# Kernel tuning notes

Measured on AMD Instinct MI355X. Metric: run time of the kernel, lower is better.

## Reference

```python
import jax, jax.numpy as jnp
import numpy as np

IN_FEATURE = 256
OUT_FEATURE = 128
ALPHA = 0.5  # LeakyReLU negative slope
NEG_BIG = -9e15


def setup_inputs() -> dict:
    key = jax.random.key(0)
    k1, k2, k3, k4 = jax.random.split(key, 4)
    N = 8192
    x = jax.random.normal(k1, (N, IN_FEATURE), dtype=jnp.float32)
    adj = jax.random.randint(k2, (N, N), 0, 2, dtype=jnp.int32)
    stdv = 1.0 / np.sqrt(OUT_FEATURE)
    W = jax.random.uniform(k3, (IN_FEATURE, OUT_FEATURE), dtype=jnp.float32,
                           minval=-stdv, maxval=stdv)
    a = jax.random.uniform(k4, (2 * OUT_FEATURE, 1), dtype=jnp.float32,
                           minval=-stdv, maxval=stdv)
    return {"input": x, "adj": adj, "W": W, "a": a}


def reference(input, adj, W, a):
    # h: [N, F_out]
    h = input @ W
    # Additive attention: cat([h_i, h_j]) @ a == h_i @ a1 + h_j @ a2
    a1 = a[:OUT_FEATURE, 0]   # [F_out]
    a2 = a[OUT_FEATURE:, 0]   # [F_out]
    f1 = h @ a1               # [N]  (row / source contribution)
    f2 = h @ a2               # [N]  (col / target contribution)
    e = jax.nn.leaky_relu(f1[:, None] + f2[None, :], negative_slope=ALPHA)  # [N, N]
    scores = jnp.where(adj > 0, e, NEG_BIG)
    attention = jax.nn.softmax(scores, axis=1)  # [N, N]
    h_prime = attention @ h                     # [N, F_out]
    return jax.nn.elu(h_prime)
```

## Files before the change

### kernel.cpp

```cpp
#include <hip/hip_runtime.h>

#define N_NODES 8192
#define IN_F 256
#define OUT_F 128
#define ALPHA 0.5f
#define JC 8
#define KCHUNK 1024
#define RK 32
#define ROUNDS 32

using short8 = __attribute__((ext_vector_type(8))) short;
using f32x4  = __attribute__((ext_vector_type(4))) float;

__device__ __forceinline__ unsigned int f2bf(float f){
  unsigned int u = __float_as_uint(f);
  u += 0x7fffu + ((u >> 16) & 1u);
  return u >> 16;
}

__device__ __forceinline__ void gld16(const void* g, void* l){
  __builtin_amdgcn_global_load_lds(
      (const __attribute__((address_space(1))) unsigned int*)g,
      (__attribute__((address_space(3))) unsigned int*)l, 16, 0, 0);
}

__global__ __launch_bounds__(256) void k_h(const float* __restrict__ x,
                                           const float* __restrict__ W,
                                           float* __restrict__ h){
  __shared__ float xs[16*IN_F];
  const int tid = threadIdx.x;
  const int r0 = blockIdx.x * 16;
  const float4* xg = (const float4*)(x + (size_t)r0*IN_F);
  float4* xl = (float4*)xs;
  #pragma unroll
  for(int i=0;i<4;i++) xl[tid + i*256] = xg[tid + i*256];
  __syncthreads();
  const int wave = tid >> 6, lane = tid & 63;
  float2 acc[4];
  #pragma unroll
  for(int j=0;j<4;j++){ acc[j].x = 0.f; acc[j].y = 0.f; }
  const float2* Wp = (const float2*)W;
  for(int k4=0;k4<IN_F;k4+=4){
    float4 xq[4];
    #pragma unroll
    for(int j=0;j<4;j++) xq[j] = *(const float4*)&xs[(wave*4+j)*IN_F + k4];
    #pragma unroll
    for(int kk=0;kk<4;kk++){
      float2 wv = Wp[(size_t)(k4+kk)*64 + lane];
      #pragma unroll
      for(int j=0;j<4;j++){
        float xv = kk==0?xq[j].x : kk==1?xq[j].y : kk==2?xq[j].z : xq[j].w;
        acc[j].x += xv*wv.x; acc[j].y += xv*wv.y;
      }
    }
  }
  #pragma unroll
  for(int j=0;j<4;j++)
    *(float2*)(h + (size_t)(r0 + wave*4 + j)*OUT_F + lane*2) = acc[j];
}

__global__ __launch_bounds__(256) void k_f(const float* __restrict__ h,
                                           const float* __restrict__ a,
                                           float* __restrict__ f1,
                                           float* __restrict__ f2){
  const int wave = threadIdx.x >> 6, lane = threadIdx.x & 63;
  const int row = blockIdx.x*4 + wave;
  float2 hv = ((const float2*)(h + (size_t)row*OUT_F))[lane];
  float2 a1 = ((const float2*)a)[lane];
  float2 a2 = ((const float2*)(a + OUT_F))[lane];
  float s1 = hv.x*a1.x + hv.y*a1.y;
  float s2 = hv.x*a2.x + hv.y*a2.y;
  #pragma unroll
  for(int off=32; off; off>>=1){
    s1 += __shfl_down(s1, off);
    s2 += __shfl_down(s2, off);
  }
  if(lane == 0){ f1[row] = s1; f2[row] = s2; }
}

#define LDW 132
__global__ __launch_bounds__(256) void k_pack(const float* __restrict__ h,
                                              unsigned short* __restrict__ P){
  __shared__ float ld[32*LDW];
  const int tid = threadIdx.x;
  const int kb = blockIdx.x, j0 = kb*32;
  #pragma unroll
  for(int i=0;i<4;i++){
    int idx = tid + i*256;
    int row = idx >> 5, c4 = (idx & 31)*4;
    *(float4*)&ld[row*LDW + c4] = *(const float4*)(h + (size_t)(j0+row)*OUT_F + c4);
  }
  __syncthreads();
  #pragma unroll
  for(int i=0;i<2;i++){
    int o = tid*2 + i;
    int c = o >> 6, lane = o & 63;
    int q = lane >> 4, n = lane & 15;
    short8 v;
    #pragma unroll
    for(int t=0;t<8;t++) v[t] = (short)f2bf(ld[(q*8+t)*LDW + c*16 + n]);
    *(short8*)(P + ((size_t)(kb*8 + c)*64 + lane)*8) = v;
  }
}

__global__ __launch_bounds__(256, 2) void k_attn(const int* __restrict__ adj,
    const unsigned short* __restrict__ P,
    const float* __restrict__ f1, const float* __restrict__ f2,
    float* __restrict__ part, float* __restrict__ denp){
  __shared__ __align__(16) char Alds[2][16384];
  __shared__ __align__(16) char Blds[2][8192];
  __shared__ float f2s[KCHUNK];
  __shared__ float f1s[128];
  const int tid = threadIdx.x;
  const int wave = tid >> 6, lane = tid & 63;
  const int m = lane & 15, q = lane >> 4;
  const int jc = blockIdx.x;
  const int r0b = blockIdx.y * 128;
  const int jb = jc * KCHUNK;

  ((float4*)f2s)[tid] = ((const float4*)(f2 + jb))[tid];
  if(tid < 128) f1s[tid] = f1[r0b + tid];

  const int g = (lane & 7) ^ (lane >> 3);
  const char* asrc[4];
  #pragma unroll
  for(int i=0;i<4;i++){
    int rowid = (wave*4 + i)*8 + (lane >> 3);
    asrc[i] = (const char*)(adj + (size_t)(r0b + rowid)*N_NODES + jb) + g*16;
  }
  const char* bsrc[2];
  #pragma unroll
  for(int i=0;i<2;i++)
    bsrc[i] = (const char*)P + (size_t)jc*ROUNDS*8192 + ((size_t)(wave*2+i)*64 + lane)*16;

  auto issue_dma = [&](int rd, int buf){
    #pragma unroll
    for(int i=0;i<4;i++)
      gld16(asrc[i] + (size_t)rd*128, Alds[buf] + (wave*4+i)*1024 + lane*16);
    #pragma unroll
    for(int i=0;i<2;i++)
      gld16(bsrc[i] + (size_t)rd*8192, Blds[buf] + (wave*2+i)*1024 + lane*16);
  };

  issue_dma(0, 0);

  f32x4 acc0[8], acc1[8];
  #pragma unroll
  for(int c=0;c<8;c++){ acc0[c] = (f32x4){0,0,0,0}; acc1[c] = (f32x4){0,0,0,0}; }
  float den0 = 0.f, den1 = 0.f;

  const int rg0 = wave*32 + m;
  const int xr = m & 7;
  const int s0 = (q*2) ^ xr, s1 = s0 ^ 1;

  __syncthreads();
  const float rf1a = f1s[rg0];
  const float rf1b = f1s[rg0 + 16];

  auto wcalc = [&](int4 alo, int4 ahi, float4 fva, float4 fvb,
                   float rf1, float& den) -> short8 {
    short8 af; float t, w;
    #define WE(slot, av, fv)                              \
      t = rf1 + (fv); t = fmaxf(t, ALPHA*t);              \
      w = ((av) > 0) ? __expf(t) : 0.f;                   \
      den += w; af[slot] = (short)f2bf(w);
    WE(0,alo.x,fva.x) WE(1,alo.y,fva.y) WE(2,alo.z,fva.z) WE(3,alo.w,fva.w)
    WE(4,ahi.x,fvb.x) WE(5,ahi.y,fvb.y) WE(6,ahi.z,fvb.z) WE(7,ahi.w,fvb.w)
    #undef WE
    return af;
  };

  for(int rd=0; rd<ROUNDS; rd++){
    const int buf = rd & 1;
    if(rd+1 < ROUNDS) issue_dma(rd+1, buf ^ 1);
    const int4* Arow0 = (const int4*)(Alds[buf] + rg0*128);
    const int4* Arow1 = (const int4*)(Alds[buf] + (rg0+16)*128);
    int4 alo0 = Arow0[s0], ahi0 = Arow0[s1];
    int4 alo1 = Arow1[s0], ahi1 = Arow1[s1];
    float4 fva = *(const float4*)(f2s + rd*RK + q*8);
    float4 fvb = *(const float4*)(f2s + rd*RK + q*8 + 4);
    short8 af0 = wcalc(alo0, ahi0, fva, fvb, rf1a, den0);
    short8 af1 = wcalc(alo1, ahi1, fva, fvb, rf1b, den1);
    const short8* Bl = (const short8*)(Blds[buf]) + lane;
    #pragma unroll
    for(int c=0;c<8;c++){
      short8 Bf = Bl[c*64];
      acc0[c] = __builtin_amdgcn_mfma_f32_16x16x32_bf16(af0, Bf, acc0[c], 0,0,0);
      acc1[c] = __builtin_amdgcn_mfma_f32_16x16x32_bf16(af1, Bf, acc1[c], 0,0,0);
    }
    __syncthreads();
  }

  den0 += __shfl_down(den0, 32); den0 += __shfl_down(den0, 16);
  den1 += __shfl_down(den1, 32); den1 += __shfl_down(den1, 16);
  const int r0w = r0b + wave*32;
  if(lane < 16){
    denp[(size_t)jc*N_NODES + r0w + lane]      = den0;
    denp[(size_t)jc*N_NODES + r0w + 16 + lane] = den1;
  }
  float* pp = part + (size_t)jc*N_NODES*OUT_F;
  #pragma unroll
  for(int c=0;c<8;c++){
    #pragma unroll
    for(int reg=0;reg<4;reg++){
      pp[(size_t)(r0w + q*4 + reg)*OUT_F      + c*16 + m] = acc0[c][reg];
      pp[(size_t)(r0w + 16 + q*4 + reg)*OUT_F + c*16 + m] = acc1[c][reg];
    }
  }
}

__global__ __launch_bounds__(256) void k_out(const float* __restrict__ part,
    const float* __restrict__ denp, float* __restrict__ out){
  const int idx = blockIdx.x*256 + threadIdx.x;
  const int r = idx >> 7;
  float v = 0.f, d = 0.f;
  #pragma unroll
  for(int p=0;p<JC;p++){
    v += part[(size_t)p*N_NODES*OUT_F + idx];
    d += denp[(size_t)p*N_NODES + r];
  }
  v /= d;
  out[idx] = v > 0.f ? v : (__expf(v) - 1.f);
}

extern "C" void kernel_launch(void* const* d_in, const int* in_sizes, int n_in,
                              void* d_out, int out_size, void* d_ws, size_t ws_size,
                              hipStream_t stream){
  const float* x   = (const float*)d_in[0];
  const int*   adj = (const int*)d_in[1];
  const float* W   = (const float*)d_in[2];
  const float* a   = (const float*)d_in[3];
  char* ws = (char*)d_ws;
  float* h            = (float*)ws;
  unsigned short* P   = (unsigned short*)(ws + (4u<<20));
  float* f1           = (float*)(ws + (6u<<20));
  float* f2           = (float*)(ws + (6u<<20) + (32u<<10));
  float* part         = (float*)(ws + (8u<<20));
  float* denp         = (float*)(ws + (40u<<20));
  float* out          = (float*)d_out;

  k_h<<<512, 256, 0, stream>>>(x, W, h);
  k_f<<<2048, 256, 0, stream>>>(h, a, f1, f2);
  k_pack<<<256, 256, 0, stream>>>(h, P);
  k_attn<<<dim3(JC,64), 256, 0, stream>>>(adj, P, f1, f2, part, denp);
  k_out<<<(N_NODES*OUT_F)/256, 256, 0, stream>>>(part, denp, out);
}
```

Before: 446.5 us.

## Compress adjacency into a bitmask pre-pass and load B fragments directly to registers

A new pre-kernel reads the int32 adjacency matrix once and packs it into a 64-bit-per-row-chunk bitmask using wave ballots. The attention kernel then stages only the compact bitmask for its tile in LDS and takes mask bits per slot, instead of streaming int32 adjacency tiles through LDS with async global-to-LDS DMA. B fragments are now software-pipelined straight from global memory into registers, which removes the per-round barrier. The adjacency read is still 256 MB of mandatory traffic, now paid in a separate streaming pass, and the register prefetch raises register pressure.

```diff
diff --git a/kernel.cpp b/kernel.cpp
--- a/kernel.cpp
+++ b/kernel.cpp
@@ -6,7 +6,6 @@
 #define ALPHA 0.5f
 #define JC 8
 #define KCHUNK 1024
-#define RK 32
 #define ROUNDS 32
 
 using short8 = __attribute__((ext_vector_type(8))) short;
@@ -16,12 +15,6 @@
   unsigned int u = __float_as_uint(f);
   u += 0x7fffu + ((u >> 16) & 1u);
   return u >> 16;
-}
-
-__device__ __forceinline__ void gld16(const void* g, void* l){
-  __builtin_amdgcn_global_load_lds(
-      (const __attribute__((address_space(1))) unsigned int*)g,
-      (__attribute__((address_space(3))) unsigned int*)l, 16, 0, 0);
 }
 
 __global__ __launch_bounds__(256) void k_h(const float* __restrict__ x,
@@ -103,12 +96,34 @@
   }
 }
 
-__global__ __launch_bounds__(256, 2) void k_attn(const int* __restrict__ adj,
+__global__ __launch_bounds__(256) void k_comp(const int* __restrict__ adj,
+                                              unsigned long long* __restrict__ bm){
+  const int lane = threadIdx.x & 63;
+  const int wid = (blockIdx.x*256 + threadIdx.x) >> 6;
+  const int nw = (gridDim.x*256) >> 6;
+  const size_t total = (size_t)N_NODES*N_NODES;
+  for(size_t base = (size_t)wid*512; base < total; base += (size_t)nw*512){
+    unsigned long long msk[8];
+    #pragma unroll
+    for(int u=0;u<8;u++){
+      int v = adj[base + (size_t)u*64 + lane];
+      msk[u] = __ballot(v > 0);
+    }
+    if(lane < 8){
+      unsigned long long v = msk[0];
+      #pragma unroll
+      for(int u=1;u<8;u++) v = (lane == u) ? msk[u] : v;
+      bm[base/64 + lane] = v;
+    }
+  }
+}
+
+__global__ __launch_bounds__(256, 2) void k_attn(
+    const unsigned int* __restrict__ bmw,
     const unsigned short* __restrict__ P,
     const float* __restrict__ f1, const float* __restrict__ f2,
     float* __restrict__ part, float* __restrict__ denp){
-  __shared__ __align__(16) char Alds[2][16384];
-  __shared__ __align__(16) char Blds[2][8192];
+  __shared__ unsigned int bs[128*32];
   __shared__ float f2s[KCHUNK];
   __shared__ float f1s[128];
   const int tid = threadIdx.x;
@@ -116,79 +131,72 @@
   const int m = lane & 15, q = lane >> 4;
   const int jc = blockIdx.x;
   const int r0b = blockIdx.y * 128;
-  const int jb = jc * KCHUNK;
-
-  ((float4*)f2s)[tid] = ((const float4*)(f2 + jb))[tid];
+
+  ((float4*)f2s)[tid] = ((const float4*)(f2 + jc*KCHUNK))[tid];
   if(tid < 128) f1s[tid] = f1[r0b + tid];
-
-  const int g = (lane & 7) ^ (lane >> 3);
-  const char* asrc[4];
-  #pragma unroll
-  for(int i=0;i<4;i++){
-    int rowid = (wave*4 + i)*8 + (lane >> 3);
-    asrc[i] = (const char*)(adj + (size_t)(r0b + rowid)*N_NODES + jb) + g*16;
-  }
-  const char* bsrc[2];
-  #pragma unroll
-  for(int i=0;i<2;i++)
-    bsrc[i] = (const char*)P + (size_t)jc*ROUNDS*8192 + ((size_t)(wave*2+i)*64 + lane)*16;
-
-  auto issue_dma = [&](int rd, int buf){
-    #pragma unroll
-    for(int i=0;i<4;i++)
-      gld16(asrc[i] + (size_t)rd*128, Alds[buf] + (wave*4+i)*1024 + lane*16);
-    #pragma unroll
-    for(int i=0;i<2;i++)
-      gld16(bsrc[i] + (size_t)rd*8192, Blds[buf] + (wave*2+i)*1024 + lane*16);
-  };
-
-  issue_dma(0, 0);
+  {
+    const int row = tid >> 1, h16 = (tid & 1) * 16;
+    const unsigned int* src = bmw + (size_t)(r0b + row)*256 + jc*32 + h16;
+    const int sw = row & 31;
+    #pragma unroll
+    for(int i=0;i<16;i+=4){
+      uint4 v = *(const uint4*)(src + i);
+      bs[row*32 + ((h16+i  ) ^ sw)] = v.x;
+      bs[row*32 + ((h16+i+1) ^ sw)] = v.y;
+      bs[row*32 + ((h16+i+2) ^ sw)] = v.z;
+      bs[row*32 + ((h16+i+3) ^ sw)] = v.w;
+    }
+  }
+  __syncthreads();
+
+  const int rg0 = wave*32 + m;
+  const float rf1a = f1s[rg0], rf1b = f1s[rg0 + 16];
+  const unsigned int* bw0 = &bs[rg0*32];
+  const unsigned int* bw1 = &bs[(rg0+16)*32];
+  const int x0 = rg0 & 31, x1 = (rg0+16) & 31;
+  const short8* PB = (const short8*)P + (size_t)jc*ROUNDS*512 + lane;
 
   f32x4 acc0[8], acc1[8];
   #pragma unroll
   for(int c=0;c<8;c++){ acc0[c] = (f32x4){0,0,0,0}; acc1[c] = (f32x4){0,0,0,0}; }
   float den0 = 0.f, den1 = 0.f;
 
-  const int rg0 = wave*32 + m;
-  const int xr = m & 7;
-  const int s0 = (q*2) ^ xr, s1 = s0 ^ 1;
-
-  __syncthreads();
-  const float rf1a = f1s[rg0];
-  const float rf1b = f1s[rg0 + 16];
-
-  auto wcalc = [&](int4 alo, int4 ahi, float4 fva, float4 fvb,
+  auto wcalc = [&](unsigned int bits, float4 fa, float4 fb,
                    float rf1, float& den) -> short8 {
     short8 af; float t, w;
-    #define WE(slot, av, fv)                              \
+    #define WE(slot, fv)                                  \
       t = rf1 + (fv); t = fmaxf(t, ALPHA*t);              \
-      w = ((av) > 0) ? __expf(t) : 0.f;                   \
+      w = (bits & (1u<<(slot))) ? __expf(t) : 0.f;        \
       den += w; af[slot] = (short)f2bf(w);
-    WE(0,alo.x,fva.x) WE(1,alo.y,fva.y) WE(2,alo.z,fva.z) WE(3,alo.w,fva.w)
-    WE(4,ahi.x,fvb.x) WE(5,ahi.y,fvb.y) WE(6,ahi.z,fvb.z) WE(7,ahi.w,fvb.w)
+    WE(0,fa.x) WE(1,fa.y) WE(2,fa.z) WE(3,fa.w)
+    WE(4,fb.x) WE(5,fb.y) WE(6,fb.z) WE(7,fb.w)
     #undef WE
     return af;
   };
 
+  short8 Bf[8], Bn[8];
+  #pragma unroll
+  for(int c=0;c<8;c++) Bn[c] = PB[c*64];
+
   for(int rd=0; rd<ROUNDS; rd++){
-    const int buf = rd & 1;
-    if(rd+1 < ROUNDS) issue_dma(rd+1, buf ^ 1);
-    const int4* Arow0 = (const int4*)(Alds[buf] + rg0*128);
-    const int4* Arow1 = (const int4*)(Alds[buf] + (rg0+16)*128);
-    int4 alo0 = Arow0[s0], ahi0 = Arow0[s1];
-    int4 alo1 = Arow1[s0], ahi1 = Arow1[s1];
-    float4 fva = *(const float4*)(f2s + rd*RK + q*8);
-    float4 fvb = *(const float4*)(f2s + rd*RK + q*8 + 4);
-    short8 af0 = wcalc(alo0, ahi0, fva, fvb, rf1a, den0);
-    short8 af1 = wcalc(alo1, ahi1, fva, fvb, rf1b, den1);
-    const short8* Bl = (const short8*)(Blds[buf]) + lane;
+    #pragma unroll
+    for(int c=0;c<8;c++) Bf[c] = Bn[c];
+    if(rd+1 < ROUNDS){
+      const short8* Bq = PB + (size_t)(rd+1)*512;
+      #pragma unroll
+      for(int c=0;c<8;c++) Bn[c] = Bq[c*64];
+    }
+    unsigned int b0 = (bw0[rd ^ x0] >> (q*8)) & 0xffu;
+    unsigned int b1 = (bw1[rd ^ x1] >> (q*8)) & 0xffu;
+    float4 fva = *(const float4*)(f2s + rd*32 + q*8);
+    float4 fvb = *(const float4*)(f2s + rd*32 + q*8 + 4);
+    short8 af0 = wcalc(b0, fva, fvb, rf1a, den0);
+    short8 af1 = wcalc(b1, fva, fvb, rf1b, den1);
     #pragma unroll
     for(int c=0;c<8;c++){
-      short8 Bf = Bl[c*64];
-      acc0[c] = __builtin_amdgcn_mfma_f32_16x16x32_bf16(af0, Bf, acc0[c], 0,0,0);
-      acc1[c] = __builtin_amdgcn_mfma_f32_16x16x32_bf16(af1, Bf, acc1[c], 0,0,0);
-    }
-    __syncthreads();
+      acc0[c] = __builtin_amdgcn_mfma_f32_16x16x32_bf16(af0, Bf[c], acc0[c], 0,0,0);
+      acc1[c] = __builtin_amdgcn_mfma_f32_16x16x32_bf16(af1, Bf[c], acc1[c], 0,0,0);
+    }
   }
 
   den0 += __shfl_down(den0, 32); den0 += __shfl_down(den0, 16);
@@ -237,11 +245,13 @@
   float* f2           = (float*)(ws + (6u<<20) + (32u<<10));
   float* part         = (float*)(ws + (8u<<20));
   float* denp         = (float*)(ws + (40u<<20));
+  unsigned long long* bm = (unsigned long long*)(ws + (48u<<20));
   float* out          = (float*)d_out;
 
+  k_comp<<<2048, 256, 0, stream>>>(adj, bm);
   k_h<<<512, 256, 0, stream>>>(x, W, h);
   k_f<<<2048, 256, 0, stream>>>(h, a, f1, f2);
   k_pack<<<256, 256, 0, stream>>>(h, P);
-  k_attn<<<dim3(JC,64), 256, 0, stream>>>(adj, P, f1, f2, part, denp);
+  k_attn<<<dim3(JC,64), 256, 0, stream>>>((const unsigned int*)bm, P, f1, f2, part, denp);
   k_out<<<(N_NODES*OUT_F)/256, 256, 0, stream>>>(part, denp, out);
 }
```

Result: no change. 441.0 us (-1.2%).
